# Kernel optimization log

Measured on AMD Instinct MI355X. Metric: run time of the kernel, lower is better.

The kernel has to match this reference:

```python
import jax, jax.numpy as jnp
import numpy as np

RADIUS = 5
REG_TH = 10.0
BIG_KEY = 2**30


def setup_inputs() -> dict:
    key = jax.random.key(0)
    k1, k2, k3, k4 = jax.random.split(key, 4)
    B, L, A, R = 32, 6, 1024, 1024
    pre_hough = jax.random.normal(k1, (B, 1, A, R), dtype=jnp.float32)
    gt_hough = jax.random.uniform(k2, (B, 1, A, R), dtype=jnp.float32)
    in_pre_points = jax.random.randint(k3, (B, L, 2), 0, 1000, dtype=jnp.int32)
    gt_points = jax.random.randint(k4, (B, L, 2), 0, 1000, dtype=jnp.int32)
    return {"pre_hough": pre_hough, "gt_hough": gt_hough,
            "in_pre_points": in_pre_points, "gt_points": gt_points}


def reference(pre_hough, gt_hough, in_pre_points, gt_points):
    B, _, A, R = pre_hough.shape  # A = Angle (height), R = Rho (width)
    L = gt_points.shape[1]
    ph = jax.nn.sigmoid(pre_hough)

    # sort pre points per batch by x*10000 + y; invalid (x<0) points sort last (padding)
    px, py = in_pre_points[..., 0], in_pre_points[..., 1]
    sort_key = jnp.where(px < 0, BIG_KEY, px * 10000 + py)
    order = jnp.argsort(sort_key, axis=1)
    pre_pts = jnp.take_along_axis(in_pre_points, order[..., None], axis=1)  # [B,L,2]

    use_gt = gt_points[..., 0] >= 0
    pt = jnp.where(use_gt[..., None], gt_points, pre_pts)  # [B,L,2]
    x, y = pt[..., 0], pt[..., 1]

    offs = jnp.arange(-RADIUS, RADIUS + 1)  # 11 offsets
    xi = x[..., None] + offs  # [B,L,11] indexes Angle axis
    yi = y[..., None] + offs  # [B,L,11] indexes Rho axis
    # original bounds x by width (Rho) and y by height (Angle); here A==R so consistent
    mx = (xi >= 0) & (xi < R)
    my = (yi >= 0) & (yi < A)
    xic = jnp.clip(xi, 0, A - 1)
    yic = jnp.clip(yi, 0, R - 1)

    b = jnp.arange(B)[:, None, None, None]
    pp = ph[b, 0, xic[:, :, :, None], yic[:, :, None, :]]        # [B,L,11,11]
    gp = gt_hough[b, 0, xic[:, :, :, None], yic[:, :, None, :]]  # [B,L,11,11]
    mask = (mx[:, :, :, None] & my[:, :, None, :]).astype(ph.dtype)

    per_pt = jnp.sum(jnp.abs(pp - gp) * mask, axis=(2, 3))  # [B,L]
    one_invalid = (pre_pts[..., 0] < 0) | (gt_points[..., 0] < 0)
    both_invalid = (pre_pts[..., 0] < 0) & (gt_points[..., 0] < 0)
    per_pt = per_pt * jnp.where(one_invalid, REG_TH, 1.0) / (RADIUS * RADIUS)
    per_pt = jnp.where(both_invalid, 0.0, per_pt)

    total = jnp.sum(per_pt)
    fallback = jnp.mean(jnp.abs(ph - gt_hough))  # F.l1_loss mean when no valid points
    return jnp.where(total == 0.0, fallback, total / B)
```

## Files before the change

kernel.cpp:

```cpp
#include <hip/hip_runtime.h>

#define RADIUS 5
#define DIAM 11
#define PATCH (DIAM * DIAM)
#define B_ 32
#define L_ 6
#define A_ 1024
#define R_ 1024
#define BIG_KEY (1 << 30)
#define REG_TH 10.0f

__global__ void k_zero(float* ws) {
    ws[0] = 0.0f;
    ws[1] = 0.0f;
}

__global__ void k_total(const float* __restrict__ pre, const float* __restrict__ gt,
                        const int* __restrict__ pre_pts, const int* __restrict__ gt_pts,
                        float* ws) {
    const int bl = blockIdx.x;
    const int b = bl / L_;
    const int l = bl % L_;

    __shared__ int sx, sy;
    __shared__ float sscale;

    if (threadIdx.x == 0) {
        int px[L_], py[L_];
        long long key[L_];
        for (int i = 0; i < L_; ++i) {
            px[i] = pre_pts[(b * L_ + i) * 2 + 0];
            py[i] = pre_pts[(b * L_ + i) * 2 + 1];
            key[i] = (px[i] < 0) ? (long long)BIG_KEY
                                 : (long long)px[i] * 10000 + (long long)py[i];
        }
        int o = 0;
        for (int i = 0; i < L_; ++i) {
            int r = 0;
            for (int j = 0; j < L_; ++j)
                if (key[j] < key[i] || (key[j] == key[i] && j < i)) ++r;
            if (r == l) { o = i; break; }
        }
        const int gx = gt_pts[(b * L_ + l) * 2 + 0];
        const int gy = gt_pts[(b * L_ + l) * 2 + 1];
        const int prx = px[o], pry = py[o];
        const bool use_gt = (gx >= 0);
        sx = use_gt ? gx : prx;
        sy = use_gt ? gy : pry;
        const bool one_inv = (prx < 0) || (gx < 0);
        const bool both_inv = (prx < 0) && (gx < 0);
        sscale = both_inv ? 0.0f
                          : (one_inv ? REG_TH : 1.0f) * (1.0f / (float)(RADIUS * RADIUS));
    }
    __syncthreads();

    const int t = threadIdx.x;
    float v = 0.0f;
    if (t < PATCH) {
        const int i = t / DIAM;
        const int j = t % DIAM;
        const int xi = sx - RADIUS + i;
        const int yi = sy - RADIUS + j;
        const bool m = (xi >= 0) && (xi < R_) && (yi >= 0) && (yi < A_);
        const int xic = min(max(xi, 0), A_ - 1);
        const int yic = min(max(yi, 0), R_ - 1);
        const size_t idx = (size_t)b * (size_t)(A_ * R_) + (size_t)xic * R_ + (size_t)yic;
        const float p = 1.0f / (1.0f + expf(-pre[idx]));
        const float g = gt[idx];
        v = m ? fabsf(p - g) : 0.0f;
    }

    for (int off = 32; off > 0; off >>= 1) v += __shfl_down(v, off, 64);
    __shared__ float partial[2];
    const int wave = t >> 6;
    if ((t & 63) == 0) partial[wave] = v;
    __syncthreads();
    if (t == 0) atomicAdd(&ws[0], (partial[0] + partial[1]) * sscale);
}

__global__ void k_fallback(const float* __restrict__ pre, const float* __restrict__ gt,
                           float* ws) {
    if (ws[0] != 0.0f) return;
    const size_t N = (size_t)B_ * (size_t)(A_ * R_);
    float acc = 0.0f;
    for (size_t i = (size_t)blockIdx.x * blockDim.x + threadIdx.x; i < N;
         i += (size_t)gridDim.x * blockDim.x) {
        const float p = 1.0f / (1.0f + expf(-pre[i]));
        acc += fabsf(p - gt[i]);
    }
    for (int off = 32; off > 0; off >>= 1) acc += __shfl_down(acc, off, 64);
    __shared__ float part[4];
    const int wave = threadIdx.x >> 6;
    if ((threadIdx.x & 63) == 0) part[wave] = acc;
    __syncthreads();
    if (threadIdx.x == 0) {
        float s = 0.0f;
        for (int w = 0; w < (int)(blockDim.x >> 6); ++w) s += part[w];
        atomicAdd(&ws[1], s);
    }
}

__global__ void k_final(const float* __restrict__ ws, float* __restrict__ out) {
    const float total = ws[0];
    const float N = (float)((size_t)B_ * (size_t)(A_ * R_));
    out[0] = (total == 0.0f) ? (ws[1] / N) : (total / (float)B_);
}

extern "C" void kernel_launch(void* const* d_in, const int* in_sizes, int n_in,
                              void* d_out, int out_size, void* d_ws, size_t ws_size,
                              hipStream_t stream) {
    const float* pre = (const float*)d_in[0];
    const float* gt = (const float*)d_in[1];
    const int* prep = (const int*)d_in[2];
    const int* gtp = (const int*)d_in[3];
    float* out = (float*)d_out;
    float* ws = (float*)d_ws;

    k_zero<<<1, 1, 0, stream>>>(ws);
    k_total<<<B_ * L_, 128, 0, stream>>>(pre, gt, prep, gtp, ws);
    k_fallback<<<256, 256, 0, stream>>>(pre, gt, ws);
    k_final<<<1, 1, 0, stream>>>(ws, out);
}
```

Measured before the change: 216.8 us.

## Replace atomics with per-point partials and merge launches into two kernels

Each point block now writes its scaled partial into its own workspace slot instead of doing an atomicAdd, so the zeroing kernel is no longer needed. A single-block finish kernel reduces the 192 partials and writes the output directly. Only when the total is zero does it run the fallback full-tensor L1 mean, now in that one 256-thread block. The launch count drops from four to two, at the cost of a very slow fallback path if it is ever taken.

Measured after the change: 213.6 us. No clear change (-1.5%).

```diff
diff --git a/kernel.cpp b/kernel.cpp
--- a/kernel.cpp
+++ b/kernel.cpp
@@ -9,15 +9,11 @@
 #define R_ 1024
 #define BIG_KEY (1 << 30)
 #define REG_TH 10.0f
+#define NPTS (B_ * L_)
 
-__global__ void k_zero(float* ws) {
-    ws[0] = 0.0f;
-    ws[1] = 0.0f;
-}
-
-__global__ void k_total(const float* __restrict__ pre, const float* __restrict__ gt,
-                        const int* __restrict__ pre_pts, const int* __restrict__ gt_pts,
-                        float* ws) {
+__global__ void k_points(const float* __restrict__ pre, const float* __restrict__ gt,
+                         const int* __restrict__ pre_pts, const int* __restrict__ gt_pts,
+                         float* __restrict__ ws) {
     const int bl = blockIdx.x;
     const int b = bl / L_;
     const int l = bl % L_;
@@ -72,38 +68,40 @@
 
     for (int off = 32; off > 0; off >>= 1) v += __shfl_down(v, off, 64);
     __shared__ float partial[2];
-    const int wave = t >> 6;
-    if ((t & 63) == 0) partial[wave] = v;
+    if ((t & 63) == 0) partial[t >> 6] = v;
     __syncthreads();
-    if (t == 0) atomicAdd(&ws[0], (partial[0] + partial[1]) * sscale);
+    if (t == 0) ws[bl] = (partial[0] + partial[1]) * sscale;
 }
 
-__global__ void k_fallback(const float* __restrict__ pre, const float* __restrict__ gt,
-                           float* ws) {
-    if (ws[0] != 0.0f) return;
+__global__ void k_finish(const float* __restrict__ pre, const float* __restrict__ gt,
+                         const float* __restrict__ ws, float* __restrict__ out) {
+    const int t = threadIdx.x;
+    __shared__ float part[4];
+    __shared__ float s_total;
+
+    float v = (t < NPTS) ? ws[t] : 0.0f;
+    for (int off = 32; off > 0; off >>= 1) v += __shfl_down(v, off, 64);
+    if ((t & 63) == 0) part[t >> 6] = v;
+    __syncthreads();
+    if (t == 0) s_total = part[0] + part[1] + part[2] + part[3];
+    __syncthreads();
+    const float total = s_total;
+
+    if (total != 0.0f) {
+        if (t == 0) out[0] = total / (float)B_;
+        return;
+    }
+
     const size_t N = (size_t)B_ * (size_t)(A_ * R_);
     float acc = 0.0f;
-    for (size_t i = (size_t)blockIdx.x * blockDim.x + threadIdx.x; i < N;
-         i += (size_t)gridDim.x * blockDim.x) {
+    for (size_t i = t; i < N; i += (size_t)blockDim.x) {
         const float p = 1.0f / (1.0f + expf(-pre[i]));
         acc += fabsf(p - gt[i]);
     }
     for (int off = 32; off > 0; off >>= 1) acc += __shfl_down(acc, off, 64);
-    __shared__ float part[4];
-    const int wave = threadIdx.x >> 6;
-    if ((threadIdx.x & 63) == 0) part[wave] = acc;
+    if ((t & 63) == 0) part[t >> 6] = acc;
     __syncthreads();
-    if (threadIdx.x == 0) {
-        float s = 0.0f;
-        for (int w = 0; w < (int)(blockDim.x >> 6); ++w) s += part[w];
-        atomicAdd(&ws[1], s);
-    }
-}
-
-__global__ void k_final(const float* __restrict__ ws, float* __restrict__ out) {
-    const float total = ws[0];
-    const float N = (float)((size_t)B_ * (size_t)(A_ * R_));
-    out[0] = (total == 0.0f) ? (ws[1] / N) : (total / (float)B_);
+    if (t == 0) out[0] = (part[0] + part[1] + part[2] + part[3]) / (float)N;
 }
 
 extern "C" void kernel_launch(void* const* d_in, const int* in_sizes, int n_in,
@@ -116,8 +114,6 @@
     float* out = (float*)d_out;
     float* ws = (float*)d_ws;
 
-    k_zero<<<1, 1, 0, stream>>>(ws);
-    k_total<<<B_ * L_, 128, 0, stream>>>(pre, gt, prep, gtp, ws);
-    k_fallback<<<256, 256, 0, stream>>>(pre, gt, ws);
-    k_final<<<1, 1, 0, stream>>>(ws, out);
+    k_points<<<NPTS, 128, 0, stream>>>(pre, gt, prep, gtp, ws);
+    k_finish<<<1, 256, 0, stream>>>(pre, gt, ws, out);
 }
```
